# Kernel optimization log

Measured on AMD Instinct MI355X. Metric: run time of the kernel, lower is better.

## Reference

```python
import jax, jax.numpy as jnp
import numpy as np

NUM_NODES = 20000
NUM_EDGES = 65536
WIDTH = 64
EDGE_FEAT = 6
HIDDEN = 128


def setup_inputs() -> dict:
    key = jax.random.key(0)
    ks = jax.random.split(key, 6)
    x = jax.random.normal(ks[0], (NUM_NODES, WIDTH), dtype=jnp.float32)
    edge_attr = jax.random.normal(ks[1], (NUM_EDGES, EDGE_FEAT), dtype=jnp.float32)
    # weight-generating MLP params (the `nn` callable), fan-in scaled
    W1 = jax.random.normal(ks[2], (EDGE_FEAT, HIDDEN), dtype=jnp.float32) / np.sqrt(EDGE_FEAT)
    b1 = jnp.zeros((HIDDEN,), dtype=jnp.float32)
    W2 = jax.random.normal(ks[3], (HIDDEN, WIDTH * WIDTH), dtype=jnp.float32) / np.sqrt(HIDDEN)
    b2 = jnp.zeros((WIDTH * WIDTH,), dtype=jnp.float32)
    senders = jax.random.randint(ks[4], (NUM_EDGES,), 0, NUM_NODES)
    receivers = jax.random.randint(ks[5], (NUM_EDGES,), 0, NUM_NODES)
    return {"x": x, "edge_attr": edge_attr, "W1": W1, "b1": b1,
            "W2": W2, "b2": b2, "senders": senders, "receivers": receivers}


def reference(x, edge_attr, W1, b1, W2, b2, senders, receivers):
    n_segs, width = x.shape
    # nn(edge_attr): (E, width*width) edge-conditioned weights
    h = jax.nn.relu(edge_attr @ W1 + b1)
    weight = (h @ W2 + b2).reshape(-1, width, width)  # (E, w, w)
    # gather sender features, per-edge (1,w) @ (w,w) matmul -> (E, w)
    msgs = jnp.einsum('ew,ewv->ev', x[senders], weight)
    # scatter-sum messages into receiver nodes (aggr == 'sum')
    return jax.ops.segment_sum(msgs, receivers, num_segments=n_segs)
```

## Files before the change

### kernel.cpp

```cpp
#include <hip/hip_runtime.h>
#include <stdint.h>

typedef _Float16 f16;
typedef f16 f16x8 __attribute__((ext_vector_type(8)));
typedef float f32x4 __attribute__((ext_vector_type(4)));

#define NUM_NODES 20000
#define NUM_EDGES 65536
#define WIDTH 64
#define EDGE_FEAT 6
#define HIDDEN 128
#define BM 128
#define NCHUNK 129
#define XPAD 72
#define HPAD 130

#define XH_HALFS (NUM_NODES * WIDTH)
#define XCONV_BLKS 625
#define W2G_HALFS (NCHUNK * 4096)
#define OUT_FLOATS (NUM_NODES * WIDTH)
#define ZBLKS 313

__device__ __forceinline__ void gload_lds16(const f16* g, f16* l) {
  __builtin_amdgcn_global_load_lds(
      (const __attribute__((address_space(1))) unsigned int*)g,
      (__attribute__((address_space(3))) unsigned int*)l, 16, 0, 0);
}

__global__ __launch_bounds__(256) void prep_kernel(
    const float* __restrict__ x, const float* __restrict__ W2,
    const float* __restrict__ b2, f16* __restrict__ ws_h,
    float* __restrict__ out)
{
  f16* x_h = ws_h;
  f16* W2g = ws_h + XH_HALFS;
  const int blk = blockIdx.x, tid = threadIdx.x;

  if (blk < NCHUNK) {
    __shared__ float row[4096];
    const int ki = blk;
    const float* srcrow;
    if (ki < HIDDEN) {
      const float4* src = (const float4*)(W2 + (size_t)ki * 4096);
      #pragma unroll
      for (int i = 0; i < 4; ++i) {
        float4 v = src[tid + 256 * i];
        *(float4*)&row[(tid + 256 * i) * 4] = v;
      }
      __syncthreads();
      srcrow = row;
    } else {
      srcrow = b2;
    }
    const int obase = tid * 16;
    f16x8 outv0, outv1;
    #pragma unroll
    for (int u = 0; u < 8; ++u) {
      int o = obase + u;
      int n = o >> 6, pg = (o >> 3) & 7, j = o & 7;
      int k = (pg ^ (n & 7)) * 8 + j;
      outv0[u] = (f16)srcrow[k * 64 + n];
    }
    #pragma unroll
    for (int u = 0; u < 8; ++u) {
      int o = obase + 8 + u;
      int n = o >> 6, pg = (o >> 3) & 7, j = o & 7;
      int k = (pg ^ (n & 7)) * 8 + j;
      outv1[u] = (f16)srcrow[k * 64 + n];
    }
    *(f16x8*)&W2g[(size_t)ki * 4096 + obase] = outv0;
    *(f16x8*)&W2g[(size_t)ki * 4096 + obase + 8] = outv1;
  } else if (blk < NCHUNK + XCONV_BLKS) {
    int idx = (blk - NCHUNK) * 2048 + tid * 8;
    if (idx + 8 <= XH_HALFS) {
      float4 a = *(const float4*)(x + idx);
      float4 b = *(const float4*)(x + idx + 4);
      f16x8 hv;
      hv[0] = (f16)a.x; hv[1] = (f16)a.y; hv[2] = (f16)a.z; hv[3] = (f16)a.w;
      hv[4] = (f16)b.x; hv[5] = (f16)b.y; hv[6] = (f16)b.z; hv[7] = (f16)b.w;
      *(f16x8*)&x_h[idx] = hv;
    }
  } else {
    int base = (blk - NCHUNK - XCONV_BLKS) * 4096 + tid * 16;
    float4 z = {0.f, 0.f, 0.f, 0.f};
    #pragma unroll
    for (int i = 0; i < 4; ++i) {
      int idx = base + i * 4;
      if (idx + 4 <= OUT_FLOATS) *(float4*)(out + idx) = z;
    }
  }
}

__global__ __launch_bounds__(256, 2) void nnconv_kernel(
    const float* __restrict__ ea, const float* __restrict__ W1,
    const float* __restrict__ b1, const int* __restrict__ senders,
    const int* __restrict__ receivers, const f16* __restrict__ ws_h,
    float* __restrict__ out)
{
  const f16* x_h = ws_h;
  const f16* W2g = ws_h + XH_HALFS;
  __shared__ __align__(16) f16 xt[BM][XPAD];
  __shared__ __align__(16) f16 hbuf[HIDDEN * HPAD];
  __shared__ __align__(16) f16 ring[3 * 4096];

  const int tid = threadIdx.x;
  const int lane = tid & 63, wid = tid >> 6;
  const int quad = lane >> 4, l15 = lane & 15;
  const int mhalf = wid >> 1, nhalf = wid & 1;
  const int e0 = blockIdx.x * BM;
  const int mbase = mhalf * 64;

  const f16* wsrc = W2g + wid * 1024 + (lane << 3);
  const int stg_off = wid * 1024;

  gload_lds16(wsrc, &ring[stg_off]);
  gload_lds16(wsrc + 512, &ring[stg_off + 512]);
  gload_lds16(wsrc + 4096, &ring[4096 + stg_off]);
  gload_lds16(wsrc + 4096 + 512, &ring[4096 + stg_off + 512]);

  float* eaf = (float*)&ring[2 * 4096];
  if (tid < 192)
    ((float4*)eaf)[tid] = ((const float4*)(ea + (size_t)e0 * EDGE_FEAT))[tid];

  {
    int r = tid >> 1, half = tid & 1;
    int s = senders[e0 + r];
    const uint4* src = (const uint4*)(x_h + (size_t)s * WIDTH + half * 32);
    uint4* dst = (uint4*)&xt[r][half * 32];
    #pragma unroll
    for (int i = 0; i < 4; ++i) dst[i] = src[i];
  }

  __syncthreads();

  {
    const int k = tid >> 1, half = tid & 1;
    float b1c = b1[k];
    float w1c[6];
    #pragma unroll
    for (int f = 0; f < 6; ++f) w1c[f] = W1[f * HIDDEN + k];
    f16* hrow = &hbuf[k * HPAD + half * 64];
    const float* er = eaf + half * 64 * EDGE_FEAT;
    #pragma unroll 2
    for (int g8 = 0; g8 < 8; ++g8) {
      f16x8 hv;
      #pragma unroll
      for (int j = 0; j < 8; ++j) {
        const float* p = er + (g8 * 8 + j) * EDGE_FEAT;
        float s = b1c;
        #pragma unroll
        for (int f = 0; f < 6; ++f) s = fmaf(p[f], w1c[f], s);
        hv[j] = (f16)fmaxf(s, 0.f);
      }
      *(f16x8*)&hrow[g8 * 8] = hv;
    }
  }

  f16x8 xf[4][2];
  #pragma unroll
  for (int t = 0; t < 4; ++t)
    #pragma unroll
    for (int kc = 0; kc < 2; ++kc)
      xf[t][kc] = *(const f16x8*)&xt[mbase + t * 16 + l15][kc * 32 + quad * 8];

  int boff[2][2];
  #pragma unroll
  for (int kc = 0; kc < 2; ++kc)
    #pragma unroll
    for (int nt = 0; nt < 2; ++nt) {
      int n = nhalf * 32 + nt * 16 + l15;
      int g = kc * 4 + quad;
      boff[kc][nt] = n * 64 + (g ^ (n & 7)) * 8;
    }

  const f16* hb = &hbuf[mbase + l15];

  f32x4 acc[4][2];
  #pragma unroll
  for (int t = 0; t < 4; ++t)
    #pragma unroll
    for (int nt = 0; nt < 2; ++nt)
      acc[t][nt] = (f32x4){0.f, 0.f, 0.f, 0.f};

  __syncthreads();

#define STEP(K, SLOT, STG, SDST, VM)                                          \
  {                                                                           \
    asm volatile("s_waitcnt vmcnt(%0) lgkmcnt(0)\n\ts_barrier"                \
                 :: "i"(VM) : "memory");                                      \
    __builtin_amdgcn_sched_barrier(0);                                        \
    if (STG) {                                                                \
      const f16* s_ = wsrc + (size_t)((K) + 2) * 4096;                        \
      f16* d_ = &ring[(SDST) * 4096 + stg_off];                               \
      gload_lds16(s_, d_);                                                    \
      gload_lds16(s_ + 512, d_ + 512);                                        \
    }                                                                         \
    __builtin_amdgcn_sched_barrier(0);                                        \
    f16 hv_[4];                                                               \
    _Pragma("unroll") for (int t = 0; t < 4; ++t)                             \
      hv_[t] = hb[(K) * HPAD + t * 16];                                       \
    const f16* gb_ = &ring[(SLOT) * 4096];                                    \
    f16x8 bf_[2][2];                                                          \
    _Pragma("unroll") for (int kc = 0; kc < 2; ++kc)                          \
      _Pragma("unroll") for (int nt = 0; nt < 2; ++nt)                        \
        bf_[kc][nt] = *(const f16x8*)&gb_[boff[kc][nt]];                      \
    f16x8 sa0_[4], sa1_[4];                                                   \
    _Pragma("unroll") for (int t = 0; t < 4; ++t) {                           \
      sa0_[t] = xf[t][0] * hv_[t];                                            \
      sa1_[t] = xf[t][1] * hv_[t];                                            \
    }                                                                         \
    __builtin_amdgcn_s_setprio(1);                                            \
    _Pragma("unroll") for (int t = 0; t < 4; ++t)                             \
      _Pragma("unroll") for (int nt = 0; nt < 2; ++nt)                        \
        acc[t][nt] = __builtin_amdgcn_mfma_f32_16x16x32_f16(                  \
            sa0_[t], bf_[0][nt], acc[t][nt], 0, 0, 0);                        \
    _Pragma("unroll") for (int t = 0; t < 4; ++t)                             \
      _Pragma("unroll") for (int nt = 0; nt < 2; ++nt)                        \
        acc[t][nt] = __builtin_amdgcn_mfma_f32_16x16x32_f16(                  \
            sa1_[t], bf_[1][nt], acc[t][nt], 0, 0, 0);                        \
    __builtin_amdgcn_s_setprio(0);                                            \
  }

  #pragma unroll 1
  for (int kb = 0; kb < 126; kb += 6) {
    STEP(kb + 0, 0, 1, 2, 2);
    STEP(kb + 1, 1, 1, 0, 2);
    STEP(kb + 2, 2, 1, 1, 2);
    STEP(kb + 3, 0, 1, 2, 2);
    STEP(kb + 4, 1, 1, 0, 2);
    STEP(kb + 5, 2, 1, 1, 2);
  }
  STEP(126, 0, 1, 2, 2);
  STEP(127, 1, 0, 0, 2);

  asm volatile("s_waitcnt vmcnt(0) lgkmcnt(0)\n\ts_barrier" ::: "memory");
  __builtin_amdgcn_sched_barrier(0);
  {
    const f16* gb_ = &ring[2 * 4096];
    f16x8 bf_[2][2];
    #pragma unroll
    for (int kc = 0; kc < 2; ++kc)
      #pragma unroll
      for (int nt = 0; nt < 2; ++nt)
        bf_[kc][nt] = *(const f16x8*)&gb_[boff[kc][nt]];
    __builtin_amdgcn_s_setprio(1);
    #pragma unroll
    for (int t = 0; t < 4; ++t)
      #pragma unroll
      for (int nt = 0; nt < 2; ++nt) {
        acc[t][nt] = __builtin_amdgcn_mfma_f32_16x16x32_f16(
            xf[t][0], bf_[0][nt], acc[t][nt], 0, 0, 0);
        acc[t][nt] = __builtin_amdgcn_mfma_f32_16x16x32_f16(
            xf[t][1], bf_[1][nt], acc[t][nt], 0, 0, 0);
      }
    __builtin_amdgcn_s_setprio(0);
  }
#undef STEP

  #pragma unroll
  for (int t = 0; t < 4; ++t) {
    int ebase = e0 + mbase + t * 16 + quad * 4;
    int rc[4];
    #pragma unroll
    for (int r = 0; r < 4; ++r) rc[r] = receivers[ebase + r];
    #pragma unroll
    for (int nt = 0; nt < 2; ++nt) {
      int v = (nhalf * 2 + nt) * 16 + l15;
      #pragma unroll
      for (int r = 0; r < 4; ++r)
        atomicAdd(out + (size_t)rc[r] * WIDTH + v, acc[t][nt][r]);
    }
  }
}

extern "C" void kernel_launch(void* const* d_in, const int* in_sizes, int n_in,
                              void* d_out, int out_size, void* d_ws, size_t ws_size,
                              hipStream_t stream) {
  const float* x  = (const float*)d_in[0];
  const float* ea = (const float*)d_in[1];
  const float* W1 = (const float*)d_in[2];
  const float* b1 = (const float*)d_in[3];
  const float* W2 = (const float*)d_in[4];
  const float* b2 = (const float*)d_in[5];
  const int* snd  = (const int*)d_in[6];
  const int* rcv  = (const int*)d_in[7];
  float* out = (float*)d_out;
  f16* wsh = (f16*)d_ws;

  const int prep_grid = NCHUNK + XCONV_BLKS + ZBLKS;
  prep_kernel<<<prep_grid, 256, 0, stream>>>(x, W2, b2, wsh, out);
  nnconv_kernel<<<NUM_EDGES / BM, 256, 0, stream>>>(ea, W1, b1, snd, rcv, wsh, out);
}
```

Measured before the change: 145.7 us.

## Register double-buffer LDS B fragments and h values one step ahead

Each step now loads the next chunk's B fragments and h scalars from LDS into a second register set before issuing the current chunk's MFMAs, ping-ponging between two register buffers. The goal is to hide LDS read latency behind the matrix instructions. To keep the prefetched ring slot valid, the per-step wait becomes vmcnt(0) instead of vmcnt(2), so global-to-LDS staging is waited on sooner. This adds register pressure and may expose global load latency.

```diff
diff --git a/kernel.cpp b/kernel.cpp
--- a/kernel.cpp
+++ b/kernel.cpp
@@ -184,10 +184,19 @@
 
   __syncthreads();
 
-#define STEP(K, SLOT, STG, SDST, VM)                                          \
+  f16x8 bfA[2][2], bfB[2][2];
+  f16 hvA[4], hvB[4];
+  #pragma unroll
+  for (int kc = 0; kc < 2; ++kc)
+    #pragma unroll
+    for (int nt = 0; nt < 2; ++nt)
+      bfA[kc][nt] = *(const f16x8*)&ring[boff[kc][nt]];
+  #pragma unroll
+  for (int t = 0; t < 4; ++t) hvA[t] = hb[t * 16];
+
+#define STEP(K, CB, CH, NB, NH, RSLOT, STG, SDST)                             \
   {                                                                           \
-    asm volatile("s_waitcnt vmcnt(%0) lgkmcnt(0)\n\ts_barrier"                \
-                 :: "i"(VM) : "memory");                                      \
+    asm volatile("s_waitcnt vmcnt(0) lgkmcnt(0)\n\ts_barrier" ::: "memory");  \
     __builtin_amdgcn_sched_barrier(0);                                        \
     if (STG) {                                                                \
       const f16* s_ = wsrc + (size_t)((K) + 2) * 4096;                        \
@@ -196,66 +205,57 @@
       gload_lds16(s_ + 512, d_ + 512);                                        \
     }                                                                         \
     __builtin_amdgcn_sched_barrier(0);                                        \
-    f16 hv_[4];                                                               \
-    _Pragma("unroll") for (int t = 0; t < 4; ++t)                             \
-      hv_[t] = hb[(K) * HPAD + t * 16];                                       \
-    const f16* gb_ = &ring[(SLOT) * 4096];                                    \
-    f16x8 bf_[2][2];                                                          \
-    _Pragma("unroll") for (int kc = 0; kc < 2; ++kc)                          \
-      _Pragma("unroll") for (int nt = 0; nt < 2; ++nt)                        \
-        bf_[kc][nt] = *(const f16x8*)&gb_[boff[kc][nt]];                      \
+    {                                                                         \
+      const f16* rb_ = &ring[(RSLOT) * 4096];                                 \
+      _Pragma("unroll") for (int kc = 0; kc < 2; ++kc)                        \
+        _Pragma("unroll") for (int nt = 0; nt < 2; ++nt)                      \
+          NB[kc][nt] = *(const f16x8*)&rb_[boff[kc][nt]];                     \
+      const int hk_ = ((K) + 1 < 128) ? (K) + 1 : 127;                        \
+      _Pragma("unroll") for (int t = 0; t < 4; ++t)                           \
+        NH[t] = hb[hk_ * HPAD + t * 16];                                      \
+    }                                                                         \
+    __builtin_amdgcn_sched_barrier(0);                                        \
     f16x8 sa0_[4], sa1_[4];                                                   \
     _Pragma("unroll") for (int t = 0; t < 4; ++t) {                           \
-      sa0_[t] = xf[t][0] * hv_[t];                                            \
-      sa1_[t] = xf[t][1] * hv_[t];                                            \
+      sa0_[t] = xf[t][0] * CH[t];                                             \
+      sa1_[t] = xf[t][1] * CH[t];                                             \
     }                                                                         \
     __builtin_amdgcn_s_setprio(1);                                            \
     _Pragma("unroll") for (int t = 0; t < 4; ++t)                             \
       _Pragma("unroll") for (int nt = 0; nt < 2; ++nt)                        \
         acc[t][nt] = __builtin_amdgcn_mfma_f32_16x16x32_f16(                  \
-            sa0_[t], bf_[0][nt], acc[t][nt], 0, 0, 0);                        \
+            sa0_[t], CB[0][nt], acc[t][nt], 0, 0, 0);                         \
     _Pragma("unroll") for (int t = 0; t < 4; ++t)                             \
       _Pragma("unroll") for (int nt = 0; nt < 2; ++nt)                        \
         acc[t][nt] = __builtin_amdgcn_mfma_f32_16x16x32_f16(                  \
-            sa1_[t], bf_[1][nt], acc[t][nt], 0, 0, 0);                        \
+            sa1_[t], CB[1][nt], acc[t][nt], 0, 0, 0);                         \
     __builtin_amdgcn_s_setprio(0);                                            \
   }
 
   #pragma unroll 1
   for (int kb = 0; kb < 126; kb += 6) {
-    STEP(kb + 0, 0, 1, 2, 2);
-    STEP(kb + 1, 1, 1, 0, 2);
-    STEP(kb + 2, 2, 1, 1, 2);
-    STEP(kb + 3, 0, 1, 2, 2);
-    STEP(kb + 4, 1, 1, 0, 2);
-    STEP(kb + 5, 2, 1, 1, 2);
-  }
-  STEP(126, 0, 1, 2, 2);
-  STEP(127, 1, 0, 0, 2);
-
-  asm volatile("s_waitcnt vmcnt(0) lgkmcnt(0)\n\ts_barrier" ::: "memory");
-  __builtin_amdgcn_sched_barrier(0);
-  {
-    const f16* gb_ = &ring[2 * 4096];
-    f16x8 bf_[2][2];
-    #pragma unroll
-    for (int kc = 0; kc < 2; ++kc)
-      #pragma unroll
-      for (int nt = 0; nt < 2; ++nt)
-        bf_[kc][nt] = *(const f16x8*)&gb_[boff[kc][nt]];
-    __builtin_amdgcn_s_setprio(1);
-    #pragma unroll
-    for (int t = 0; t < 4; ++t)
-      #pragma unroll
-      for (int nt = 0; nt < 2; ++nt) {
-        acc[t][nt] = __builtin_amdgcn_mfma_f32_16x16x32_f16(
-            xf[t][0], bf_[0][nt], acc[t][nt], 0, 0, 0);
-        acc[t][nt] = __builtin_amdgcn_mfma_f32_16x16x32_f16(
-            xf[t][1], bf_[1][nt], acc[t][nt], 0, 0, 0);
-      }
-    __builtin_amdgcn_s_setprio(0);
-  }
+    STEP(kb + 0, bfA, hvA, bfB, hvB, 1, 1, 2);
+    STEP(kb + 1, bfB, hvB, bfA, hvA, 2, 1, 0);
+    STEP(kb + 2, bfA, hvA, bfB, hvB, 0, 1, 1);
+    STEP(kb + 3, bfB, hvB, bfA, hvA, 1, 1, 2);
+    STEP(kb + 4, bfA, hvA, bfB, hvB, 2, 1, 0);
+    STEP(kb + 5, bfB, hvB, bfA, hvA, 0, 1, 1);
+  }
+  STEP(126, bfA, hvA, bfB, hvB, 1, 1, 2);
+  STEP(127, bfB, hvB, bfA, hvA, 2, 0, 0);
 #undef STEP
+
+  __builtin_amdgcn_s_setprio(1);
+  #pragma unroll
+  for (int t = 0; t < 4; ++t)
+    #pragma unroll
+    for (int nt = 0; nt < 2; ++nt) {
+      acc[t][nt] = __builtin_amdgcn_mfma_f32_16x16x32_f16(
+          xf[t][0], bfA[0][nt], acc[t][nt], 0, 0, 0);
+      acc[t][nt] = __builtin_amdgcn_mfma_f32_16x16x32_f16(
+          xf[t][1], bfA[1][nt], acc[t][nt], 0, 0, 0);
+    }
+  __builtin_amdgcn_s_setprio(0);
 
   #pragma unroll
   for (int t = 0; t < 4; ++t) {
```

Measured after the change: 167.3 us. 1.15x slower.

## Give each wave a private double-buffered W2 ring and drop per-step block barriers

Applied to the files above, without the earlier changes.

The shared triple-buffered W2 ring, which needed a block-wide s_barrier every k step, is replaced by a per-wave double buffer. Each wave loads its own N-half of each W2 chunk and only waits on its own vmcnt, so waves no longer synchronise with each other during the main loop. In exchange, the two waves that share an N-half now fetch the same W2 data, which doubles global/L2 traffic for W2. Prefetch depth also drops to one chunk ahead. LDS padding on the x tile and the h buffer is removed, and the x gather moves after the h computation, which may add LDS bank conflicts.

```diff
diff --git a/kernel.cpp b/kernel.cpp
--- a/kernel.cpp
+++ b/kernel.cpp
@@ -12,8 +12,6 @@
 #define HIDDEN 128
 #define BM 128
 #define NCHUNK 129
-#define XPAD 72
-#define HPAD 130
 
 #define XH_HALFS (NUM_NODES * WIDTH)
 #define XCONV_BLKS 625
@@ -99,9 +97,9 @@
 {
   const f16* x_h = ws_h;
   const f16* W2g = ws_h + XH_HALFS;
-  __shared__ __align__(16) f16 xt[BM][XPAD];
-  __shared__ __align__(16) f16 hbuf[HIDDEN * HPAD];
-  __shared__ __align__(16) f16 ring[3 * 4096];
+  __shared__ __align__(16) f16 xt[BM][64];
+  __shared__ __align__(16) f16 hbuf[HIDDEN * 128];
+  __shared__ __align__(16) f16 ring[4 * 2 * 2048];
 
   const int tid = threadIdx.x;
   const int lane = tid & 63, wid = tid >> 6;
@@ -110,27 +108,9 @@
   const int e0 = blockIdx.x * BM;
   const int mbase = mhalf * 64;
 
-  const f16* wsrc = W2g + wid * 1024 + (lane << 3);
-  const int stg_off = wid * 1024;
-
-  gload_lds16(wsrc, &ring[stg_off]);
-  gload_lds16(wsrc + 512, &ring[stg_off + 512]);
-  gload_lds16(wsrc + 4096, &ring[4096 + stg_off]);
-  gload_lds16(wsrc + 4096 + 512, &ring[4096 + stg_off + 512]);
-
-  float* eaf = (float*)&ring[2 * 4096];
+  float* eaf = (float*)&xt[0][0];
   if (tid < 192)
     ((float4*)eaf)[tid] = ((const float4*)(ea + (size_t)e0 * EDGE_FEAT))[tid];
-
-  {
-    int r = tid >> 1, half = tid & 1;
-    int s = senders[e0 + r];
-    const uint4* src = (const uint4*)(x_h + (size_t)s * WIDTH + half * 32);
-    uint4* dst = (uint4*)&xt[r][half * 32];
-    #pragma unroll
-    for (int i = 0; i < 4; ++i) dst[i] = src[i];
-  }
-
   __syncthreads();
 
   {
@@ -139,7 +119,7 @@
     float w1c[6];
     #pragma unroll
     for (int f = 0; f < 6; ++f) w1c[f] = W1[f * HIDDEN + k];
-    f16* hrow = &hbuf[k * HPAD + half * 64];
+    f16* hrow = &hbuf[k * 128 + half * 64];
     const float* er = eaf + half * 64 * EDGE_FEAT;
     #pragma unroll 2
     for (int g8 = 0; g8 < 8; ++g8) {
@@ -155,6 +135,22 @@
       *(f16x8*)&hrow[g8 * 8] = hv;
     }
   }
+  __syncthreads();
+
+  {
+    int r = tid >> 1, half = tid & 1;
+    int s = senders[e0 + r];
+    const uint4* src = (const uint4*)(x_h + (size_t)s * WIDTH + half * 32);
+    uint4* dst = (uint4*)&xt[r][half * 32];
+    #pragma unroll
+    for (int i = 0; i < 4; ++i) dst[i] = src[i];
+  }
+  f16* myring = &ring[wid * 4096];
+  const f16* wsl = W2g + nhalf * 2048 + (lane << 3);
+  #pragma unroll
+  for (int i = 0; i < 4; ++i)
+    gload_lds16(wsl + i * 512, myring + i * 512);
+  __syncthreads();
 
   f16x8 xf[4][2];
   #pragma unroll
@@ -168,9 +164,9 @@
   for (int kc = 0; kc < 2; ++kc)
     #pragma unroll
     for (int nt = 0; nt < 2; ++nt) {
-      int n = nhalf * 32 + nt * 16 + l15;
+      int np = nt * 16 + l15;
       int g = kc * 4 + quad;
-      boff[kc][nt] = n * 64 + (g ^ (n & 7)) * 8;
+      boff[kc][nt] = np * 64 + (g ^ (np & 7)) * 8;
     }
 
   const f16* hb = &hbuf[mbase + l15];
@@ -182,80 +178,73 @@
     for (int nt = 0; nt < 2; ++nt)
       acc[t][nt] = (f32x4){0.f, 0.f, 0.f, 0.f};
 
-  __syncthreads();
-
-#define STEP(K, SLOT, STG, SDST, VM)                                          \
-  {                                                                           \
-    asm volatile("s_waitcnt vmcnt(%0) lgkmcnt(0)\n\ts_barrier"                \
-                 :: "i"(VM) : "memory");                                      \
-    __builtin_amdgcn_sched_barrier(0);                                        \
-    if (STG) {                                                                \
-      const f16* s_ = wsrc + (size_t)((K) + 2) * 4096;                        \
-      f16* d_ = &ring[(SDST) * 4096 + stg_off];                               \
-      gload_lds16(s_, d_);                                                    \
-      gload_lds16(s_ + 512, d_ + 512);                                        \
-    }                                                                         \
-    __builtin_amdgcn_sched_barrier(0);                                        \
-    f16 hv_[4];                                                               \
-    _Pragma("unroll") for (int t = 0; t < 4; ++t)                             \
-      hv_[t] = hb[(K) * HPAD + t * 16];                                       \
-    const f16* gb_ = &ring[(SLOT) * 4096];                                    \
-    f16x8 bf_[2][2];                                                          \
-    _Pragma("unroll") for (int kc = 0; kc < 2; ++kc)                          \
-      _Pragma("unroll") for (int nt = 0; nt < 2; ++nt)                        \
-        bf_[kc][nt] = *(const f16x8*)&gb_[boff[kc][nt]];                      \
-    f16x8 sa0_[4], sa1_[4];                                                   \
-    _Pragma("unroll") for (int t = 0; t < 4; ++t) {                           \
-      sa0_[t] = xf[t][0] * hv_[t];                                            \
-      sa1_[t] = xf[t][1] * hv_[t];                                            \
-    }                                                                         \
-    __builtin_amdgcn_s_setprio(1);                                            \
-    _Pragma("unroll") for (int t = 0; t < 4; ++t)                             \
-      _Pragma("unroll") for (int nt = 0; nt < 2; ++nt)                        \
-        acc[t][nt] = __builtin_amdgcn_mfma_f32_16x16x32_f16(                  \
-            sa0_[t], bf_[0][nt], acc[t][nt], 0, 0, 0);                        \
-    _Pragma("unroll") for (int t = 0; t < 4; ++t)                             \
-      _Pragma("unroll") for (int nt = 0; nt < 2; ++nt)                        \
-        acc[t][nt] = __builtin_amdgcn_mfma_f32_16x16x32_f16(                  \
-            sa1_[t], bf_[1][nt], acc[t][nt], 0, 0, 0);                        \
-    __builtin_amdgcn_s_setprio(0);                                            \
-  }
-
-  #pragma unroll 1
-  for (int kb = 0; kb < 126; kb += 6) {
-    STEP(kb + 0, 0, 1, 2, 2);
-    STEP(kb + 1, 1, 1, 0, 2);
-    STEP(kb + 2, 2, 1, 1, 2);
-    STEP(kb + 3, 0, 1, 2, 2);
-    STEP(kb + 4, 1, 1, 0, 2);
-    STEP(kb + 5, 2, 1, 1, 2);
-  }
-  STEP(126, 0, 1, 2, 2);
-  STEP(127, 1, 0, 0, 2);
-
-  asm volatile("s_waitcnt vmcnt(0) lgkmcnt(0)\n\ts_barrier" ::: "memory");
+  #pragma unroll 2
+  for (int k = 0; k < 128; ++k) {
+    asm volatile("s_waitcnt vmcnt(0)" ::: "memory");
+    __builtin_amdgcn_sched_barrier(0);
+    {
+      const f16* src = wsl + (size_t)(k + 1) * 4096;
+      f16* dst = myring + ((k + 1) & 1) * 2048;
+      #pragma unroll
+      for (int i = 0; i < 4; ++i)
+        gload_lds16(src + i * 512, dst + i * 512);
+    }
+    __builtin_amdgcn_sched_barrier(0);
+
+    const f16* gb = myring + (k & 1) * 2048;
+    f16x8 bf[2][2];
+    #pragma unroll
+    for (int kc = 0; kc < 2; ++kc)
+      #pragma unroll
+      for (int nt = 0; nt < 2; ++nt)
+        bf[kc][nt] = *(const f16x8*)&gb[boff[kc][nt]];
+    f16 hv[4];
+    #pragma unroll
+    for (int t = 0; t < 4; ++t) hv[t] = hb[k * 128 + t * 16];
+
+    f16x8 sa0[4], sa1[4];
+    #pragma unroll
+    for (int t = 0; t < 4; ++t) {
+      sa0[t] = xf[t][0] * hv[t];
+      sa1[t] = xf[t][1] * hv[t];
+    }
+    __builtin_amdgcn_s_setprio(1);
+    #pragma unroll
+    for (int t = 0; t < 4; ++t)
+      #pragma unroll
+      for (int nt = 0; nt < 2; ++nt)
+        acc[t][nt] = __builtin_amdgcn_mfma_f32_16x16x32_f16(
+            sa0[t], bf[0][nt], acc[t][nt], 0, 0, 0);
+    #pragma unroll
+    for (int t = 0; t < 4; ++t)
+      #pragma unroll
+      for (int nt = 0; nt < 2; ++nt)
+        acc[t][nt] = __builtin_amdgcn_mfma_f32_16x16x32_f16(
+            sa1[t], bf[1][nt], acc[t][nt], 0, 0, 0);
+    __builtin_amdgcn_s_setprio(0);
+  }
+
+  asm volatile("s_waitcnt vmcnt(0)" ::: "memory");
   __builtin_amdgcn_sched_barrier(0);
   {
-    const f16* gb_ = &ring[2 * 4096];
-    f16x8 bf_[2][2];
+    f16x8 bf[2][2];
     #pragma unroll
     for (int kc = 0; kc < 2; ++kc)
       #pragma unroll
       for (int nt = 0; nt < 2; ++nt)
-        bf_[kc][nt] = *(const f16x8*)&gb_[boff[kc][nt]];
+        bf[kc][nt] = *(const f16x8*)&myring[boff[kc][nt]];
     __builtin_amdgcn_s_setprio(1);
     #pragma unroll
     for (int t = 0; t < 4; ++t)
       #pragma unroll
       for (int nt = 0; nt < 2; ++nt) {
         acc[t][nt] = __builtin_amdgcn_mfma_f32_16x16x32_f16(
-            xf[t][0], bf_[0][nt], acc[t][nt], 0, 0, 0);
-        acc[t][nt] = __builtin_amdgcn_mfma_f32_16x16x32_f16(
-            xf[t][1], bf_[1][nt], acc[t][nt], 0, 0, 0);
+            xf[t][0], bf[0][nt], acc[t][nt], 0, 0, 0);
+        acc[t][nt] = __builtin_amdgcn_mfma_f32_16x16x32_f16(
+            xf[t][1], bf[1][nt], acc[t][nt], 0, 0, 0);
       }
     __builtin_amdgcn_s_setprio(0);
   }
-#undef STEP
 
   #pragma unroll
   for (int t = 0; t < 4; ++t) {
```

New measurement: 150.3 us. 3.1% more time.

## Fuse prep and NNConv kernels with grid-wide atomic barrier, convert x on gather

Applied to the files above, without the earlier changes.

Merges the prep kernel into the main kernel. Some blocks now transform W2 and others zero the output, and all blocks meet at a software grid barrier built on an atomic counter before the edge computation starts. The separate x-to-fp16 conversion pass is dropped, and sender rows are read as fp32 and converted while being gathered into LDS. This removes one kernel launch and a full pass over x, at the cost of a spin barrier. That barrier relies on all 512 blocks being co-resident (2 per CU) and adds a memset launch to reset the counter.

```diff
diff --git a/kernel.cpp b/kernel.cpp
--- a/kernel.cpp
+++ b/kernel.cpp
@@ -14,12 +14,10 @@
 #define NCHUNK 129
 #define XPAD 72
 #define HPAD 130
-
-#define XH_HALFS (NUM_NODES * WIDTH)
-#define XCONV_BLKS 625
+#define GRID_BLKS (NUM_EDGES / BM)
+
 #define W2G_HALFS (NCHUNK * 4096)
 #define OUT_FLOATS (NUM_NODES * WIDTH)
-#define ZBLKS 313
 
 __device__ __forceinline__ void gload_lds16(const f16* g, f16* l) {
   __builtin_amdgcn_global_load_lds(
@@ -27,17 +25,25 @@
       (__attribute__((address_space(3))) unsigned int*)l, 16, 0, 0);
 }
 
-__global__ __launch_bounds__(256) void prep_kernel(
-    const float* __restrict__ x, const float* __restrict__ W2,
-    const float* __restrict__ b2, f16* __restrict__ ws_h,
-    float* __restrict__ out)
+__global__ __launch_bounds__(256, 2) void fused_kernel(
+    const float* __restrict__ x, const float* __restrict__ ea,
+    const float* __restrict__ W1, const float* __restrict__ b1,
+    const float* __restrict__ W2, const float* __restrict__ b2,
+    const int* __restrict__ senders, const int* __restrict__ receivers,
+    f16* __restrict__ ws_h, float* __restrict__ out)
 {
-  f16* x_h = ws_h;
-  f16* W2g = ws_h + XH_HALFS;
-  const int blk = blockIdx.x, tid = threadIdx.x;
+  f16* W2g = ws_h;
+  unsigned int* ctr = (unsigned int*)(ws_h + W2G_HALFS);
+
+  __shared__ __align__(16) f16 xt[BM][XPAD];
+  __shared__ __align__(16) f16 hbuf[HIDDEN * HPAD];
+  __shared__ __align__(16) f16 ring[3 * 4096];
+
+  const int tid = threadIdx.x;
+  const int blk = blockIdx.x;
 
   if (blk < NCHUNK) {
-    __shared__ float row[4096];
+    float* row = (float*)&hbuf[0];
     const int ki = blk;
     const float* srcrow;
     if (ki < HIDDEN) {
@@ -70,44 +76,36 @@
     }
     *(f16x8*)&W2g[(size_t)ki * 4096 + obase] = outv0;
     *(f16x8*)&W2g[(size_t)ki * 4096 + obase + 8] = outv1;
-  } else if (blk < NCHUNK + XCONV_BLKS) {
-    int idx = (blk - NCHUNK) * 2048 + tid * 8;
-    if (idx + 8 <= XH_HALFS) {
-      float4 a = *(const float4*)(x + idx);
-      float4 b = *(const float4*)(x + idx + 4);
-      f16x8 hv;
-      hv[0] = (f16)a.x; hv[1] = (f16)a.y; hv[2] = (f16)a.z; hv[3] = (f16)a.w;
-      hv[4] = (f16)b.x; hv[5] = (f16)b.y; hv[6] = (f16)b.z; hv[7] = (f16)b.w;
-      *(f16x8*)&x_h[idx] = hv;
-    }
+    __syncthreads();
   } else {
-    int base = (blk - NCHUNK - XCONV_BLKS) * 4096 + tid * 16;
-    float4 z = {0.f, 0.f, 0.f, 0.f};
-    #pragma unroll
-    for (int i = 0; i < 4; ++i) {
-      int idx = base + i * 4;
-      if (idx + 4 <= OUT_FLOATS) *(float4*)(out + idx) = z;
-    }
-  }
-}
-
-__global__ __launch_bounds__(256, 2) void nnconv_kernel(
-    const float* __restrict__ ea, const float* __restrict__ W1,
-    const float* __restrict__ b1, const int* __restrict__ senders,
-    const int* __restrict__ receivers, const f16* __restrict__ ws_h,
-    float* __restrict__ out)
-{
-  const f16* x_h = ws_h;
-  const f16* W2g = ws_h + XH_HALFS;
-  __shared__ __align__(16) f16 xt[BM][XPAD];
-  __shared__ __align__(16) f16 hbuf[HIDDEN * HPAD];
-  __shared__ __align__(16) f16 ring[3 * 4096];
-
-  const int tid = threadIdx.x;
+    for (int i = blk - NCHUNK; i < 313; i += GRID_BLKS - NCHUNK) {
+      int base = i * 4096 + tid * 16;
+      float4 z = {0.f, 0.f, 0.f, 0.f};
+      #pragma unroll
+      for (int u = 0; u < 4; ++u) {
+        int idx = base + u * 4;
+        if (idx + 4 <= OUT_FLOATS) *(float4*)(out + idx) = z;
+      }
+    }
+  }
+
+  __threadfence();
+  __syncthreads();
+  if (tid == 0) {
+    __hip_atomic_fetch_add(ctr, 1u, __ATOMIC_ACQ_REL, __HIP_MEMORY_SCOPE_AGENT);
+    while (__hip_atomic_load(ctr, __ATOMIC_ACQUIRE, __HIP_MEMORY_SCOPE_AGENT)
+           < (unsigned)GRID_BLKS) {
+      __builtin_amdgcn_s_sleep(8);
+    }
+  }
+  __syncthreads();
+  __threadfence();
+  __builtin_amdgcn_sched_barrier(0);
+
   const int lane = tid & 63, wid = tid >> 6;
   const int quad = lane >> 4, l15 = lane & 15;
   const int mhalf = wid >> 1, nhalf = wid & 1;
-  const int e0 = blockIdx.x * BM;
+  const int e0 = blk * BM;
   const int mbase = mhalf * 64;
 
   const f16* wsrc = W2g + wid * 1024 + (lane << 3);
@@ -125,10 +123,17 @@
   {
     int r = tid >> 1, half = tid & 1;
     int s = senders[e0 + r];
-    const uint4* src = (const uint4*)(x_h + (size_t)s * WIDTH + half * 32);
-    uint4* dst = (uint4*)&xt[r][half * 32];
-    #pragma unroll
-    for (int i = 0; i < 4; ++i) dst[i] = src[i];
+    const float4* src = (const float4*)(x + (size_t)s * WIDTH + half * 32);
+    f16* dst = &xt[r][half * 32];
+    #pragma unroll
+    for (int i = 0; i < 4; ++i) {
+      float4 a = src[2 * i];
+      float4 b = src[2 * i + 1];
+      f16x8 hv;
+      hv[0] = (f16)a.x; hv[1] = (f16)a.y; hv[2] = (f16)a.z; hv[3] = (f16)a.w;
+      hv[4] = (f16)b.x; hv[5] = (f16)b.y; hv[6] = (f16)b.z; hv[7] = (f16)b.w;
+      *(f16x8*)&dst[i * 8] = hv;
+    }
   }
 
   __syncthreads();
@@ -287,7 +292,7 @@
   float* out = (float*)d_out;
   f16* wsh = (f16*)d_ws;
 
-  const int prep_grid = NCHUNK + XCONV_BLKS + ZBLKS;
-  prep_kernel<<<prep_grid, 256, 0, stream>>>(x, W2, b2, wsh, out);
-  nnconv_kernel<<<NUM_EDGES / BM, 256, 0, stream>>>(ea, W1, b1, snd, rcv, wsh, out);
+  hipMemsetAsync(wsh + W2G_HALFS, 0, 4, stream);
+  fused_kernel<<<GRID_BLKS, 256, 0, stream>>>(
+      x, ea, W1, b1, W2, b2, snd, rcv, wsh, out);
 }
```

New measurement: 270.8 us. +85.8%, slower.
